# Kernel tuning notes

Measured on AMD Instinct MI355X. Metric: run time of the kernel, lower is better.

The kernel has to match this reference:

```python
import jax, jax.numpy as jnp
import numpy as np

NEG_INF = -jnp.inf
EPS = 1e-12  # F.normalize eps


def _build_spans(text_mask_row, max_span_length):
    # text_mask_row: concrete bool array [S]. Returns static numpy span index arrays.
    pos = np.nonzero(np.asarray(text_mask_row))[0]
    n = pos.size
    starts, ends, lens = [], [], []
    for i in range(n):
        for j in range(i, min(i + max_span_length, n)):
            starts.append(pos[i]); ends.append(pos[j]); lens.append(j - i + 1)
    return (np.asarray(starts, np.int32), np.asarray(ends, np.int32), np.asarray(lens, np.int32))


def setup_inputs() -> dict:
    key = jax.random.key(0)
    ks = jax.random.split(key, 8)
    B, S, H, T = 16, 1024, 768, 64
    L, LE = 4, 32
    Din = 3 * H + LE
    return {
        "hidden_states": jax.random.normal(ks[0], (B, S, H), jnp.float32),
        "topic_hidden": jax.random.normal(ks[1], (B, T, H), jnp.float32),
        "topic_mask": jnp.ones((B, T), jnp.bool_),
        "text_mask": jnp.ones((B, S), jnp.bool_),
        "len_emb": jax.random.normal(ks[2], (L + 1, LE), jnp.float32) * 0.02,
        "W1": jax.random.normal(ks[3], (Din, H), jnp.float32) / np.sqrt(Din),
        "b1": jnp.zeros((H,), jnp.float32),
        "W2": jax.random.normal(ks[4], (H, H), jnp.float32) / np.sqrt(H),
        "b2": jnp.zeros((H,), jnp.float32),
    }


def _l2norm(x):
    n = jnp.sqrt(jnp.sum(x * x, axis=-1, keepdims=True))
    return x / jnp.maximum(n, EPS)


def reference(hidden_states, topic_hidden, topic_mask, text_mask, len_emb, W1, b1, W2, b2):
    B, S, H = hidden_states.shape
    max_span_length = len_emb.shape[0] - 1
    # Masks are identical across the batch (all ones here): build spans once.
    starts_np, ends_np, lens_np = _build_spans(text_mask[0], max_span_length)
    starts = jnp.asarray(starts_np); ends = jnp.asarray(ends_np); lens = jnp.asarray(lens_np)
    N = starts.shape[0]

    start_v = hidden_states[:, starts]          # [B,N,H] gather span starts
    end_v = hidden_states[:, ends]              # [B,N,H] gather span ends
    csum = jnp.concatenate([jnp.zeros((B, 1, H), hidden_states.dtype),
                            jnp.cumsum(hidden_states, axis=1)], axis=1)  # [B,S+1,H]
    mean_v = (csum[:, ends + 1] - csum[:, starts]) / lens[None, :, None].astype(hidden_states.dtype)
    len_v = jnp.broadcast_to(len_emb[lens][None], (B, N, len_emb.shape[1]))

    feat = jnp.concatenate([start_v, end_v, mean_v, len_v], axis=-1)  # [B,N,3H+LE]
    span_vec = jax.nn.gelu(feat @ W1 + b1, approximate=False) @ W2 + b2  # [B,N,H]
    span_vec = _l2norm(span_vec)
    topic_vec = _l2norm(topic_hidden)                                    # [B,T,H]

    sim = jnp.einsum('bth,bnh->btn', topic_vec, span_vec)                # [B,T,N]
    sim = jnp.where(topic_mask[:, :, None], sim, NEG_INF)
    span_scores = jnp.max(sim, axis=1)                                   # [B,N]

    tok = jnp.arange(S)
    cover = (tok[None, :] >= starts[:, None]) & (tok[None, :] <= ends[:, None])  # [N,S]
    token_scores = jnp.max(jnp.where(cover[None], span_scores[:, :, None], NEG_INF), axis=1)  # [B,S]
    token_scores = jnp.where(text_mask, token_scores, NEG_INF)
    return token_scores
```

## Files before the change

kernel.cpp:

```cpp
#include <hip/hip_runtime.h>
#include <hip/hip_bf16.h>
#include <math.h>

typedef __bf16 bf16s;
typedef __attribute__((ext_vector_type(8))) __bf16 bf16x8;
typedef __attribute__((ext_vector_type(4))) __bf16 bf16x4;
typedef __attribute__((ext_vector_type(4))) float f32x4;

#define B_   16
#define S_   1024
#define H_   768
#define T_   64
#define L_   4
#define LE_  32
#define NPAD 4096
#define BS   (B_*S_)
#define BNR  (B_*NPAD)
#define N3   (3*H_)

static __device__ __forceinline__ void gload_lds16(const void* g, void* l) {
  __builtin_amdgcn_global_load_lds(
      (const __attribute__((address_space(1))) void*)g,
      (__attribute__((address_space(3))) void*)l, 16, 0, 0);
}

__global__ __launch_bounds__(1024) void k_build_spans(
    const int* __restrict__ text_mask,
    int* __restrict__ R, int* __restrict__ pos, int* __restrict__ spoff,
    int* __restrict__ starts, int* __restrict__ ends, int* __restrict__ lens,
    int* __restrict__ meta)
{
  __shared__ int buf[S_];
  int t = threadIdx.x;
  int m = text_mask[t] ? 1 : 0;
  buf[t] = m;
  __syncthreads();
  for (int off = 1; off < S_; off <<= 1) {
    int v = buf[t];
    if (t >= off) v += buf[t - off];
    __syncthreads();
    buf[t] = v;
    __syncthreads();
  }
  int incl = buf[t];
  R[t] = incl;
  if (m) pos[incl - 1] = t;
  int n = buf[S_ - 1];
  __syncthreads();
  int cnt = (t < n) ? min(L_, n - t) : 0;
  buf[t] = cnt;
  __syncthreads();
  for (int off = 1; off < S_; off <<= 1) {
    int v = buf[t];
    if (t >= off) v += buf[t - off];
    __syncthreads();
    buf[t] = v;
    __syncthreads();
  }
  int inc2 = buf[t];
  int base = inc2 - cnt;
  spoff[t] = base;
  if (t == 0) { meta[0] = buf[S_ - 1]; meta[1] = n; }
  __syncthreads();
  if (t < n) {
    int p0 = pos[t];
    for (int k = 0; k < cnt; k++) {
      starts[base + k] = p0;
      ends[base + k]   = pos[t + k];
      lens[base + k]   = k + 1;
    }
  }
}

__global__ __launch_bounds__(256) void k_cast_bf16(const float* __restrict__ src,
                                                   bf16s* __restrict__ dst, int n4) {
  int i = blockIdx.x * 256 + threadIdx.x;
  if (i >= n4) return;
  f32x4 v = ((const f32x4*)src)[i];
  bf16x4 o;
  o[0] = (__bf16)v[0]; o[1] = (__bf16)v[1]; o[2] = (__bf16)v[2]; o[3] = (__bf16)v[3];
  ((bf16x4*)dst)[i] = o;
}

__global__ __launch_bounds__(256) void k_zero(float* __restrict__ p, int n4) {
  int i = blockIdx.x * 256 + threadIdx.x;
  if (i < n4) ((f32x4*)p)[i] = (f32x4){0.f, 0.f, 0.f, 0.f};
}

__global__ __launch_bounds__(256) void k_transpose_cast(const float* __restrict__ in,
                                                        bf16s* __restrict__ out) {
  __shared__ float tile[64][65];
  int r0 = blockIdx.x * 64, c0 = blockIdx.y * 64;
  int t = threadIdx.x;
  int tr = t >> 4;
  int tc = (t & 15) * 4;
#pragma unroll
  for (int i = 0; i < 4; i++) {
    int row = tr + i * 16;
    f32x4 v = *(const f32x4*)(in + (long)(r0 + row) * H_ + c0 + tc);
    tile[row][tc+0] = v[0]; tile[row][tc+1] = v[1];
    tile[row][tc+2] = v[2]; tile[row][tc+3] = v[3];
  }
  __syncthreads();
#pragma unroll
  for (int i = 0; i < 4; i++) {
    int cc = tr + i * 16;
    bf16x4 o;
    o[0] = (__bf16)tile[tc+0][cc]; o[1] = (__bf16)tile[tc+1][cc];
    o[2] = (__bf16)tile[tc+2][cc]; o[3] = (__bf16)tile[tc+3][cc];
    *(bf16x4*)(out + (long)(c0 + cc) * H_ + r0 + tc) = o;
  }
}

__global__ __launch_bounds__(256) void k_lt(const float* __restrict__ len_emb,
                                            const float* __restrict__ W1,
                                            float* __restrict__ LT) {
  int idx = blockIdx.x * 256 + threadIdx.x;
  if (idx >= (L_ + 1) * H_) return;
  int l = idx / H_, h = idx % H_;
  float acc = 0.f;
#pragma unroll
  for (int e = 0; e < LE_; e++) acc += len_emb[l * LE_ + e] * W1[(long)(N3 + e) * H_ + h];
  LT[idx] = acc;
}

#define BKT 64
#define GEMM_CORE_BODY(A_, Bt_, K_) \
  int tid = threadIdx.x; \
  int wid = tid >> 6, l = tid & 63; \
  int wr = wid >> 2, wc = wid & 3; \
  int srow = tid >> 3; \
  int sslot = (tid & 7) ^ (srow & 7); \
  const bf16s* gA = (A_) + (a0 + srow) * (long)(K_) + sslot * 8; \
  const bf16s* gB = (Bt_) + (b0 + srow) * (long)(K_) + sslot * 8; \
  const char* aP0 = sA + wr * 16384; \
  const char* aP1 = aP0 + 32768; \
  const char* bP0 = sB + (wc >> 1) * 16384 + (wc & 1) * 8192; \
  const char* bP1 = bP0 + 32768; \
  int lrow = (l & 15) * 128; \
  int ls0 = (((l >> 4) ^ (l & 7)) * 16); \
  f32x4 acc[8][4]; \
  _Pragma("unroll") \
  for (int i = 0; i < 8; i++) \
    _Pragma("unroll") \
    for (int j = 0; j < 4; j++) acc[i][j] = (f32x4){0.f, 0.f, 0.f, 0.f}; \
  int NT = (K_) / BKT; \
  int NITER = NT / 2; \
  STG_B(0, 0); STG_B(0, 1); STG_A(0, 0); STG_A(0, 1); \
  STG_B(1, 0); STG_B(1, 1); STG_A(1, 0); \
  asm volatile("s_waitcnt vmcnt(6)" ::: "memory"); \
  __builtin_amdgcn_s_barrier(); \
  for (int it = 0; it < NITER; ++it) { \
    int t0 = 2 * it, t1 = t0 + 1; \
    bool nl = (it != NITER - 1); \
    bf16x8 af0[4][2], af1[4][2], bfv[4][2]; \
    _Pragma("unroll") \
    for (int f = 0; f < 4; ++f) { \
      af0[f][0] = *(const bf16x8*)(aP0 + f * 2048 + lrow + ls0); \
      af0[f][1] = *(const bf16x8*)(aP0 + f * 2048 + lrow + (ls0 ^ 64)); \
    } \
    _Pragma("unroll") \
    for (int c = 0; c < 4; ++c) { \
      bfv[c][0] = *(const bf16x8*)(bP0 + c * 2048 + lrow + ls0); \
      bfv[c][1] = *(const bf16x8*)(bP0 + c * 2048 + lrow + (ls0 ^ 64)); \
    } \
    STG_A(t1, 1); \
    PH_PRE(); \
    MFMA_Q(af0, 0, 0); MFMA_Q(af0, 0, 1); \
    PH_POST(); \
    if (nl) STG_B(t0 + 2, 0); \
    PH_PRE(); \
    MFMA_Q(af0, 0, 2); MFMA_Q(af0, 0, 3); \
    PH_POST(); \
    _Pragma("unroll") \
    for (int f = 0; f < 4; ++f) { \
      af1[f][0] = *(const bf16x8*)(aP0 + (f + 4) * 2048 + lrow + ls0); \
      af1[f][1] = *(const bf16x8*)(aP0 + (f + 4) * 2048 + lrow + (ls0 ^ 64)); \
    } \
    if (nl) STG_B(t0 + 2, 1); \
    PH_PRE(); \
    MFMA_Q(af1, 4, 0); MFMA_Q(af1, 4, 1); \
    PH_POST(); \
    if (nl) { STG_A(t0 + 2, 0); asm volatile("s_waitcnt vmcnt(6)" ::: "memory"); } \
    else    { asm volatile("s_waitcnt vmcnt(0)" ::: "memory"); } \
    PH_PRE(); \
    MFMA_Q(af1, 4, 2); MFMA_Q(af1, 4, 3); \
    PH_POST(); \
    _Pragma("unroll") \
    for (int f = 0; f < 4; ++f) { \
      af0[f][0] = *(const bf16x8*)(aP1 + f * 2048 + lrow + ls0); \
      af0[f][1] = *(const bf16x8*)(aP1 + f * 2048 + lrow + (ls0 ^ 64)); \
    } \
    _Pragma("unroll") \
    for (int c = 0; c < 4; ++c) { \
      bfv[c][0] = *(const bf16x8*)(bP1 + c * 2048 + lrow + ls0); \
      bfv[c][1] = *(const bf16x8*)(bP1 + c * 2048 + lrow + (ls0 ^ 64)); \
    } \
    if (nl) STG_A(t0 + 2, 1); \
    PH_PRE(); \
    MFMA_Q(af0, 0, 0); MFMA_Q(af0, 0, 1); \
    PH_POST(); \
    if (nl) STG_B(t1 + 2, 0); \
    PH_PRE(); \
    MFMA_Q(af0, 0, 2); MFMA_Q(af0, 0, 3); \
    PH_POST(); \
    _Pragma("unroll") \
    for (int f = 0; f < 4; ++f) { \
      af1[f][0] = *(const bf16x8*)(aP1 + (f + 4) * 2048 + lrow + ls0); \
      af1[f][1] = *(const bf16x8*)(aP1 + (f + 4) * 2048 + lrow + (ls0 ^ 64)); \
    } \
    if (nl) STG_B(t1 + 2, 1); \
    PH_PRE(); \
    MFMA_Q(af1, 4, 0); MFMA_Q(af1, 4, 1); \
    PH_POST(); \
    if (nl) { STG_A(t1 + 2, 0); asm volatile("s_waitcnt vmcnt(6)" ::: "memory"); } \
    else    { asm volatile("s_waitcnt vmcnt(0)" ::: "memory"); } \
    PH_PRE(); \
    MFMA_Q(af1, 4, 2); MFMA_Q(af1, 4, 3); \
    PH_POST(); \
  }

#define STG_A(kt_, h_) do { \
    const bf16s* s_ = gA + (long)(h_) * 128 * K + (long)(kt_) * BKT; \
    char* d_ = sA + ((kt_) & 1) * 32768 + (h_) * 16384 + wid * 1024; \
    gload_lds16(s_, d_); \
    gload_lds16(s_ + 64L * K, d_ + 8192); \
  } while (0)
#define STG_B(kt_, h_) do { \
    const bf16s* s_ = gB + (long)(h_) * 128 * K + (long)(kt_) * BKT; \
    char* d_ = sB + ((kt_) & 1) * 32768 + (h_) * 16384 + wid * 1024; \
    gload_lds16(s_, d_); \
    gload_lds16(s_ + 64L * K, d_ + 8192); \
  } while (0)
#define MFMA_Q(AF_, FR0_, FC_) do { \
    _Pragma("unroll") \
    for (int f_ = 0; f_ < 4; ++f_) { \
      acc[FR0_+f_][FC_] = __builtin_amdgcn_mfma_f32_16x16x32_bf16(bfv[FC_][0], AF_[f_][0], acc[FR0_+f_][FC_], 0, 0, 0); \
      acc[FR0_+f_][FC_] = __builtin_amdgcn_mfma_f32_16x16x32_bf16(bfv[FC_][1], AF_[f_][1], acc[FR0_+f_][FC_], 0, 0, 0); \
    } } while (0)
#define PH_PRE()  __builtin_amdgcn_s_barrier(); \
                  asm volatile("s_waitcnt lgkmcnt(0)" ::: "memory"); \
                  __builtin_amdgcn_s_setprio(1)
#define PH_POST() __builtin_amdgcn_s_setprio(0); \
                  __builtin_amdgcn_s_barrier()

__global__ __launch_bounds__(512, 2) void k_gemm8p(
    const bf16s* __restrict__ A, const bf16s* __restrict__ Bt,
    bf16s* __restrict__ C, int N, int K, int NTN)
{
  __shared__ __align__(16) char sA[65536];
  __shared__ __align__(16) char sB[65536];
  int nwg = gridDim.x, bid = blockIdx.x;
  int q = nwg >> 3, rr = nwg & 7;
  int xcd = bid & 7, ix = bid >> 3;
  int nid = (xcd < rr ? xcd * (q + 1) : rr * (q + 1) + (xcd - rr) * q) + ix;
  long a0 = (long)(nid / NTN) * 256;
  long b0 = (long)(nid % NTN) * 256;

  GEMM_CORE_BODY(A, Bt, K)

#pragma unroll
  for (int half = 0; half < 2; ++half) {
    if (wr == half) {
#pragma unroll
      for (int fc = 0; fc < 4; ++fc) {
        int col2 = (wc * 64 + fc * 16 + (l >> 4) * 4) * 2;
#pragma unroll
        for (int fr = 0; fr < 8; ++fr) {
          int row_l = fr * 16 + (l & 15);
          bf16x4 o;
#pragma unroll
          for (int r = 0; r < 4; ++r) o[r] = (__bf16)acc[fr][fc][r];
          *(bf16x4*)(sA + ((row_l * 512 + col2) ^ ((row_l & 7) << 4))) = o;
        }
      }
    }
    __syncthreads();
#pragma unroll
    for (int i = 0; i < 8; ++i) {
      int off = i * 8192 + tid * 16;
      int row_l = off >> 9;
      bf16x8 v = *(const bf16x8*)(sA + (off ^ ((row_l & 7) << 4)));
      *(bf16x8*)(C + (a0 + half * 128 + row_l) * (long)N + b0 + ((off & 511) >> 1)) = v;
    }
    __syncthreads();
  }
}

__global__ __launch_bounds__(512, 2) void k_gemmnorm(
    const bf16s* __restrict__ A, const bf16s* __restrict__ Bt,
    const float* __restrict__ bias, float* __restrict__ ssbuf,
    int K, int NTN)
{
  __shared__ __align__(16) char sA[65536];
  __shared__ __align__(16) char sB[65536];
  int nwg = gridDim.x, bid = blockIdx.x;
  int q = nwg >> 3, rr = nwg & 7;
  int xcd = bid & 7, ix = bid >> 3;
  int nid = (xcd < rr ? xcd * (q + 1) : rr * (q + 1) + (xcd - rr) * q) + ix;
  long a0 = (long)(nid / NTN) * 256;
  long b0 = (long)(nid % NTN) * 256;

  GEMM_CORE_BODY(A, Bt, K)

  f32x4 bb[4];
#pragma unroll
  for (int fc = 0; fc < 4; ++fc)
    bb[fc] = *(const f32x4*)(bias + b0 + wc * 64 + fc * 16 + (l >> 4) * 4);
#pragma unroll
  for (int fr = 0; fr < 8; ++fr) {
    float p = 0.f;
#pragma unroll
    for (int fc = 0; fc < 4; ++fc)
#pragma unroll
      for (int r = 0; r < 4; ++r) {
        float y = acc[fr][fc][r] + bb[fc][r];
        p += y * y;
      }
    p += __shfl_xor(p, 16);
    p += __shfl_xor(p, 32);
    if (l < 16) atomicAdd(&ssbuf[a0 + wr * 128 + fr * 16 + l], p);
  }
}

#undef STG_A
#undef STG_B
#undef MFMA_Q
#undef PH_PRE
#undef PH_POST

__global__ __launch_bounds__(256) void k_z1(
    const bf16s* __restrict__ P,
    const float* __restrict__ LT, const float* __restrict__ b1,
    const int* __restrict__ starts, const int* __restrict__ ends,
    const int* __restrict__ lens, const int* __restrict__ meta,
    bf16s* __restrict__ X)
{
  int idx = blockIdx.x * 256 + threadIdx.x;
  int h4 = idx % (H_ / 4); int rest = idx / (H_ / 4);
  int nid = rest % NPAD; int b = rest / NPAD;
  int h = h4 * 4;
  int N = meta[0];
  long orow = (long)(b * NPAD + nid) * H_ + h;
  if (nid >= N) {
    bf16x4 z; z[0] = z[1] = z[2] = z[3] = (__bf16)0.f;
    *(bf16x4*)(X + orow) = z;
    return;
  }
  int sa = starts[nid], se = ends[nid], ln = lens[nid];
  float il = 1.0f / (float)ln;
  bf16x4 vs = *(const bf16x4*)(P + (long)(b * S_ + sa) * N3 + h);
  bf16x4 ve = *(const bf16x4*)(P + (long)(b * S_ + se) * N3 + H_ + h);
  float mv[4] = {0.f, 0.f, 0.f, 0.f};
  for (int i = sa; i <= se; i++) {
    bf16x4 vc = *(const bf16x4*)(P + (long)(b * S_ + i) * N3 + 2 * H_ + h);
#pragma unroll
    for (int j = 0; j < 4; j++) mv[j] += (float)vc[j];
  }
  f32x4 lt = *(const f32x4*)(LT + (long)ln * H_ + h);
  f32x4 bb = *(const f32x4*)(b1 + h);
  bf16x4 o;
#pragma unroll
  for (int j = 0; j < 4; j++) {
    float x = (float)vs[j] + (float)ve[j] + mv[j] * il + lt[j] + bb[j];
    float g = 0.5f * x * (1.0f + erff(x * 0.70710678118654752f));
    o[j] = (__bf16)g;
  }
  *(bf16x4*)(X + orow) = o;
}

__global__ __launch_bounds__(256) void k_topicn(const float* __restrict__ TH,
                                                const float* __restrict__ b2,
                                                bf16s* __restrict__ TN,
                                                float* __restrict__ cvec) {
  __shared__ float red[256];
  int r = blockIdx.x; int t = threadIdx.x;
  const float* row = TH + (long)r * H_;
  float v0 = row[t], v1 = row[t + 256], v2 = row[t + 512];
  red[t] = v0 * v0 + v1 * v1 + v2 * v2;
  __syncthreads();
  for (int off = 128; off; off >>= 1) {
    if (t < off) red[t] += red[t + off];
    __syncthreads();
  }
  float rn = 1.0f / fmaxf(sqrtf(red[0]), 1e-12f);
  bf16s* o = TN + (long)r * H_;
  o[t] = (__bf16)(v0 * rn); o[t + 256] = (__bf16)(v1 * rn); o[t + 512] = (__bf16)(v2 * rn);
  __syncthreads();
  red[t] = v0 * b2[t] + v1 * b2[t + 256] + v2 * b2[t + 512];
  __syncthreads();
  for (int off = 128; off; off >>= 1) {
    if (t < off) red[t] += red[t + off];
    __syncthreads();
  }
  if (t == 0) cvec[r] = red[0] * rn;
}

__global__ __launch_bounds__(256) void k_simx(
    const bf16s* __restrict__ X, const bf16s* __restrict__ U,
    const float* __restrict__ cvec, const float* __restrict__ ssbuf,
    const int* __restrict__ tmask, float* __restrict__ scores)
{
  int b = blockIdx.y;
  int wid = threadIdx.x >> 6, l = threadIdx.x & 63;
  int st = blockIdx.x * 4 + wid;
  int span = st * 16 + (l & 15);
  const bf16s* xrow = X + (long)(b * NPAD + span) * H_ + (l >> 4) * 8;
  const bf16s* ubase = U + (long)b * T_ * H_ + (l >> 4) * 8;
  f32x4 acc[4];
#pragma unroll
  for (int tt = 0; tt < 4; tt++) acc[tt] = (f32x4){0.f, 0.f, 0.f, 0.f};
  for (int kk = 0; kk < H_ / 32; kk++) {
    bf16x8 av = *(const bf16x8*)(xrow + kk * 32);
#pragma unroll
    for (int tt = 0; tt < 4; tt++) {
      bf16x8 bv = *(const bf16x8*)(ubase + (long)(tt * 16 + (l & 15)) * H_ + kk * 32);
      acc[tt] = __builtin_amdgcn_mfma_f32_16x16x32_bf16(av, bv, acc[tt], 0, 0, 0);
    }
  }
  const int* tm = tmask + b * T_;
  bool msk[4];
  float cv[4];
#pragma unroll
  for (int tt = 0; tt < 4; tt++) {
    int tcol = tt * 16 + (l & 15);
    msk[tt] = tm[tcol] != 0;
    cv[tt] = cvec[b * T_ + tcol];
  }
  float best[4];
#pragma unroll
  for (int r = 0; r < 4; r++) {
    float v = -INFINITY;
#pragma unroll
    for (int tt = 0; tt < 4; tt++) if (msk[tt]) v = fmaxf(v, acc[tt][r] + cv[tt]);
    best[r] = v;
  }
#pragma unroll
  for (int off = 8; off; off >>= 1)
#pragma unroll
    for (int r = 0; r < 4; r++) best[r] = fmaxf(best[r], __shfl_xor(best[r], off));
  if ((l & 15) == 0) {
    int srow = st * 16 + (l >> 4) * 4;
#pragma unroll
    for (int r = 0; r < 4; r++) {
      float ss = ssbuf[b * NPAD + srow + r];
      scores[b * NPAD + srow + r] = best[r] / fmaxf(sqrtf(ss), 1e-12f);
    }
  }
}

__global__ __launch_bounds__(256) void k_token(
    const int* __restrict__ text_mask,
    const int* __restrict__ R, const int* __restrict__ spoff,
    const int* __restrict__ meta, const float* __restrict__ scores,
    float* __restrict__ out)
{
  int idx = blockIdx.x * 256 + threadIdx.x;
  int s = idx % S_, b = idx / S_;
  if (!text_mask[b * S_ + s]) { out[idx] = -INFINITY; return; }
  int n = meta[1];
  int r1 = R[s];
  int le = r1 - 1;
  int ge = text_mask[s] ? (r1 - 1) : r1;
  float best = -INFINITY;
  if (le >= 0 && ge < n) {
    int i0 = max(0, ge - (L_ - 1));
    for (int i = i0; i <= le; i++) {
      int jmax = min(i + L_ - 1, n - 1);
      int off = spoff[i];
      for (int j = max(i, ge); j <= jmax; j++)
        best = fmaxf(best, scores[b * NPAD + off + (j - i)]);
    }
  }
  out[idx] = best;
}

__global__ __launch_bounds__(256) void k_sentinel(float* __restrict__ out) {
  int i = blockIdx.x * 256 + threadIdx.x;
  if (i < BS) out[i] = 12345.0f;
}

extern "C" void kernel_launch(void* const* d_in, const int* in_sizes, int n_in,
                              void* d_out, int out_size, void* d_ws, size_t ws_size,
                              hipStream_t stream) {
  const float* hid = (const float*)d_in[0];
  const float* th  = (const float*)d_in[1];
  const int* tmask = (const int*)d_in[2];
  const int* xmask = (const int*)d_in[3];
  const float* lemb = (const float*)d_in[4];
  const float* W1   = (const float*)d_in[5];
  const float* b1   = (const float*)d_in[6];
  const float* W2   = (const float*)d_in[7];
  const float* b2   = (const float*)d_in[8];
  float* out = (float*)d_out;

  char* w = (char*)d_ws;
  auto alloc = [&](size_t bytes) {
    char* p = w; w += (bytes + 255) & ~(size_t)255; return p;
  };
  bf16s* wbt   = (bf16s*)alloc((size_t)N3 * H_ * 2);
  bf16s* w2t   = (bf16s*)alloc((size_t)H_ * H_ * 2);
  bf16s* w2c   = (bf16s*)alloc((size_t)H_ * H_ * 2);
  float* LT    = (float*)alloc((size_t)(L_ + 1) * H_ * 4);
  bf16s* topn  = (bf16s*)alloc((size_t)B_ * T_ * H_ * 2);
  bf16s* U     = (bf16s*)alloc((size_t)B_ * T_ * H_ * 2);
  float* cvec  = (float*)alloc((size_t)B_ * T_ * 4);
  float* ssbuf = (float*)alloc((size_t)BNR * 4);
  float* scores= (float*)alloc((size_t)B_ * NPAD * 4);
  int* R       = (int*)alloc(S_ * 4);
  int* pos     = (int*)alloc(S_ * 4);
  int* spoff   = (int*)alloc(S_ * 4);
  int* starts  = (int*)alloc(NPAD * 4);
  int* ends    = (int*)alloc(NPAD * 4);
  int* lens    = (int*)alloc(NPAD * 4);
  int* meta    = (int*)alloc(2 * 4);
  char* regionA = alloc((size_t)BS * H_ * 2 + (size_t)BS * N3 * 2);
  bf16s* hidb  = (bf16s*)regionA;
  bf16s* P     = (bf16s*)(regionA + (size_t)BS * H_ * 2);
  bf16s* X     = (bf16s*)alloc((size_t)BNR * H_ * 2);

  size_t required = (size_t)(w - (char*)d_ws);
  if (required > ws_size) {
    k_sentinel<<<(BS + 255) / 256, 256, 0, stream>>>(out);
    return;
  }

  k_build_spans<<<1, 1024, 0, stream>>>(xmask, R, pos, spoff, starts, ends, lens, meta);
  k_cast_bf16<<<(BS * H_ / 4 + 255) / 256, 256, 0, stream>>>(hid, hidb, BS * H_ / 4);
  for (int c = 0; c < 3; c++)
    k_transpose_cast<<<dim3(12, 12), 256, 0, stream>>>(W1 + (size_t)c * H_ * H_, wbt + (size_t)c * H_ * H_);
  k_transpose_cast<<<dim3(12, 12), 256, 0, stream>>>(W2, w2t);
  k_cast_bf16<<<(H_ * H_ / 4 + 255) / 256, 256, 0, stream>>>(W2, w2c, H_ * H_ / 4);
  k_lt<<<((L_ + 1) * H_ + 255) / 256, 256, 0, stream>>>(lemb, W1, LT);
  k_zero<<<(BNR / 4 + 255) / 256, 256, 0, stream>>>(ssbuf, BNR / 4);

  k_gemm8p<<<(BS / 256) * (N3 / 256), 512, 0, stream>>>(hidb, wbt, P, N3, H_, N3 / 256);

  k_z1<<<(B_ * NPAD * (H_ / 4)) / 256, 256, 0, stream>>>(P, LT, b1, starts, ends, lens, meta, X);

  k_topicn<<<B_ * T_, 256, 0, stream>>>(th, b2, topn, cvec);
  k_gemm8p<<<(B_ * T_ / 256) * (H_ / 256), 512, 0, stream>>>(topn, w2c, U, H_, H_, H_ / 256);

  k_gemmnorm<<<(BNR / 256) * (H_ / 256), 512, 0, stream>>>(X, w2t, b2, ssbuf, H_, H_ / 256);

  k_simx<<<dim3(NPAD / 64, B_), 256, 0, stream>>>(X, U, cvec, ssbuf, tmask, scores);
  k_token<<<(B_ * S_) / 256, 256, 0, stream>>>(xmask, R, spoff, meta, scores, out);
  (void)in_sizes; (void)n_in; (void)out_size;
}
```

Measured before the change: 348.2 us.

## Merge prep kernels, chain GEMM column tiles per block, drop atomics and zeroing

New measurement: 322.1 us. -7.5%, faster.

```diff
diff --git a/kernel.cpp b/kernel.cpp
--- a/kernel.cpp
+++ b/kernel.cpp
@@ -72,162 +72,95 @@
   }
 }
 
-__global__ __launch_bounds__(256) void k_cast_bf16(const float* __restrict__ src,
-                                                   bf16s* __restrict__ dst, int n4) {
-  int i = blockIdx.x * 256 + threadIdx.x;
-  if (i >= n4) return;
-  f32x4 v = ((const f32x4*)src)[i];
-  bf16x4 o;
-  o[0] = (__bf16)v[0]; o[1] = (__bf16)v[1]; o[2] = (__bf16)v[2]; o[3] = (__bf16)v[3];
-  ((bf16x4*)dst)[i] = o;
-}
-
-__global__ __launch_bounds__(256) void k_zero(float* __restrict__ p, int n4) {
-  int i = blockIdx.x * 256 + threadIdx.x;
-  if (i < n4) ((f32x4*)p)[i] = (f32x4){0.f, 0.f, 0.f, 0.f};
-}
-
-__global__ __launch_bounds__(256) void k_transpose_cast(const float* __restrict__ in,
-                                                        bf16s* __restrict__ out) {
+__global__ __launch_bounds__(256) void k_prep(
+    const float* __restrict__ hid, bf16s* __restrict__ hidb,
+    const float* __restrict__ W1, bf16s* __restrict__ wbt,
+    const float* __restrict__ W2, bf16s* __restrict__ w2t, bf16s* __restrict__ w2c,
+    const float* __restrict__ lemb, float* __restrict__ LT,
+    const float* __restrict__ TH, const float* __restrict__ b2,
+    bf16s* __restrict__ TN, float* __restrict__ cvec)
+{
   __shared__ float tile[64][65];
-  int r0 = blockIdx.x * 64, c0 = blockIdx.y * 64;
+  __shared__ float red[256];
+  int bid = blockIdx.x;
   int t = threadIdx.x;
-  int tr = t >> 4;
-  int tc = (t & 15) * 4;
-#pragma unroll
-  for (int i = 0; i < 4; i++) {
-    int row = tr + i * 16;
-    f32x4 v = *(const f32x4*)(in + (long)(r0 + row) * H_ + c0 + tc);
-    tile[row][tc+0] = v[0]; tile[row][tc+1] = v[1];
-    tile[row][tc+2] = v[2]; tile[row][tc+3] = v[3];
-  }
-  __syncthreads();
-#pragma unroll
-  for (int i = 0; i < 4; i++) {
-    int cc = tr + i * 16;
+  if (bid < 12288) {
+    int i = bid * 256 + t;
+    f32x4 v = ((const f32x4*)hid)[i];
     bf16x4 o;
-    o[0] = (__bf16)tile[tc+0][cc]; o[1] = (__bf16)tile[tc+1][cc];
-    o[2] = (__bf16)tile[tc+2][cc]; o[3] = (__bf16)tile[tc+3][cc];
-    *(bf16x4*)(out + (long)(c0 + cc) * H_ + r0 + tc) = o;
-  }
-}
-
-__global__ __launch_bounds__(256) void k_lt(const float* __restrict__ len_emb,
-                                            const float* __restrict__ W1,
-                                            float* __restrict__ LT) {
-  int idx = blockIdx.x * 256 + threadIdx.x;
-  if (idx >= (L_ + 1) * H_) return;
-  int l = idx / H_, h = idx % H_;
-  float acc = 0.f;
-#pragma unroll
-  for (int e = 0; e < LE_; e++) acc += len_emb[l * LE_ + e] * W1[(long)(N3 + e) * H_ + h];
-  LT[idx] = acc;
+    o[0] = (__bf16)v[0]; o[1] = (__bf16)v[1]; o[2] = (__bf16)v[2]; o[3] = (__bf16)v[3];
+    ((bf16x4*)hidb)[i] = o;
+  } else if (bid < 12864) {
+    int local = bid - 12288;
+    int c = local / 144, rem = local % 144;
+    const float* in = (c < 3) ? (W1 + (size_t)c * H_ * H_) : W2;
+    bf16s* out = (c < 3) ? (wbt + (size_t)c * H_ * H_) : w2t;
+    int r0 = (rem / 12) * 64, c0 = (rem % 12) * 64;
+    int tr = t >> 4, tc = (t & 15) * 4;
+#pragma unroll
+    for (int i = 0; i < 4; i++) {
+      int row = tr + i * 16;
+      f32x4 v = *(const f32x4*)(in + (long)(r0 + row) * H_ + c0 + tc);
+      tile[row][tc+0] = v[0]; tile[row][tc+1] = v[1];
+      tile[row][tc+2] = v[2]; tile[row][tc+3] = v[3];
+    }
+    __syncthreads();
+#pragma unroll
+    for (int i = 0; i < 4; i++) {
+      int cc = tr + i * 16;
+      bf16x4 o;
+      o[0] = (__bf16)tile[tc+0][cc]; o[1] = (__bf16)tile[tc+1][cc];
+      o[2] = (__bf16)tile[tc+2][cc]; o[3] = (__bf16)tile[tc+3][cc];
+      *(bf16x4*)(out + (long)(c0 + cc) * H_ + r0 + tc) = o;
+    }
+  } else if (bid < 13440) {
+    int i = (bid - 12864) * 256 + t;
+    f32x4 v = ((const f32x4*)W2)[i];
+    bf16x4 o;
+    o[0] = (__bf16)v[0]; o[1] = (__bf16)v[1]; o[2] = (__bf16)v[2]; o[3] = (__bf16)v[3];
+    ((bf16x4*)w2c)[i] = o;
+  } else if (bid < 13455) {
+    int idx = (bid - 13440) * 256 + t;
+    if (idx < (L_ + 1) * H_) {
+      int l = idx / H_, h = idx % H_;
+      float acc = 0.f;
+#pragma unroll
+      for (int e = 0; e < LE_; e++) acc += lemb[l * LE_ + e] * W1[(long)(N3 + e) * H_ + h];
+      LT[idx] = acc;
+    }
+  } else {
+    int r = bid - 13455;
+    const float* row = TH + (long)r * H_;
+    float v0 = row[t], v1 = row[t + 256], v2 = row[t + 512];
+    red[t] = v0 * v0 + v1 * v1 + v2 * v2;
+    __syncthreads();
+    for (int off = 128; off; off >>= 1) {
+      if (t < off) red[t] += red[t + off];
+      __syncthreads();
+    }
+    float rn = 1.0f / fmaxf(sqrtf(red[0]), 1e-12f);
+    bf16s* o = TN + (long)r * H_;
+    o[t] = (__bf16)(v0 * rn); o[t + 256] = (__bf16)(v1 * rn); o[t + 512] = (__bf16)(v2 * rn);
+    __syncthreads();
+    red[t] = v0 * b2[t] + v1 * b2[t + 256] + v2 * b2[t + 512];
+    __syncthreads();
+    for (int off = 128; off; off >>= 1) {
+      if (t < off) red[t] += red[t + off];
+      __syncthreads();
+    }
+    if (t == 0) cvec[r] = red[0] * rn;
+  }
 }
 
 #define BKT 64
-#define GEMM_CORE_BODY(A_, Bt_, K_) \
-  int tid = threadIdx.x; \
-  int wid = tid >> 6, l = tid & 63; \
-  int wr = wid >> 2, wc = wid & 3; \
-  int srow = tid >> 3; \
-  int sslot = (tid & 7) ^ (srow & 7); \
-  const bf16s* gA = (A_) + (a0 + srow) * (long)(K_) + sslot * 8; \
-  const bf16s* gB = (Bt_) + (b0 + srow) * (long)(K_) + sslot * 8; \
-  const char* aP0 = sA + wr * 16384; \
-  const char* aP1 = aP0 + 32768; \
-  const char* bP0 = sB + (wc >> 1) * 16384 + (wc & 1) * 8192; \
-  const char* bP1 = bP0 + 32768; \
-  int lrow = (l & 15) * 128; \
-  int ls0 = (((l >> 4) ^ (l & 7)) * 16); \
-  f32x4 acc[8][4]; \
-  _Pragma("unroll") \
-  for (int i = 0; i < 8; i++) \
-    _Pragma("unroll") \
-    for (int j = 0; j < 4; j++) acc[i][j] = (f32x4){0.f, 0.f, 0.f, 0.f}; \
-  int NT = (K_) / BKT; \
-  int NITER = NT / 2; \
-  STG_B(0, 0); STG_B(0, 1); STG_A(0, 0); STG_A(0, 1); \
-  STG_B(1, 0); STG_B(1, 1); STG_A(1, 0); \
-  asm volatile("s_waitcnt vmcnt(6)" ::: "memory"); \
-  __builtin_amdgcn_s_barrier(); \
-  for (int it = 0; it < NITER; ++it) { \
-    int t0 = 2 * it, t1 = t0 + 1; \
-    bool nl = (it != NITER - 1); \
-    bf16x8 af0[4][2], af1[4][2], bfv[4][2]; \
-    _Pragma("unroll") \
-    for (int f = 0; f < 4; ++f) { \
-      af0[f][0] = *(const bf16x8*)(aP0 + f * 2048 + lrow + ls0); \
-      af0[f][1] = *(const bf16x8*)(aP0 + f * 2048 + lrow + (ls0 ^ 64)); \
-    } \
-    _Pragma("unroll") \
-    for (int c = 0; c < 4; ++c) { \
-      bfv[c][0] = *(const bf16x8*)(bP0 + c * 2048 + lrow + ls0); \
-      bfv[c][1] = *(const bf16x8*)(bP0 + c * 2048 + lrow + (ls0 ^ 64)); \
-    } \
-    STG_A(t1, 1); \
-    PH_PRE(); \
-    MFMA_Q(af0, 0, 0); MFMA_Q(af0, 0, 1); \
-    PH_POST(); \
-    if (nl) STG_B(t0 + 2, 0); \
-    PH_PRE(); \
-    MFMA_Q(af0, 0, 2); MFMA_Q(af0, 0, 3); \
-    PH_POST(); \
-    _Pragma("unroll") \
-    for (int f = 0; f < 4; ++f) { \
-      af1[f][0] = *(const bf16x8*)(aP0 + (f + 4) * 2048 + lrow + ls0); \
-      af1[f][1] = *(const bf16x8*)(aP0 + (f + 4) * 2048 + lrow + (ls0 ^ 64)); \
-    } \
-    if (nl) STG_B(t0 + 2, 1); \
-    PH_PRE(); \
-    MFMA_Q(af1, 4, 0); MFMA_Q(af1, 4, 1); \
-    PH_POST(); \
-    if (nl) { STG_A(t0 + 2, 0); asm volatile("s_waitcnt vmcnt(6)" ::: "memory"); } \
-    else    { asm volatile("s_waitcnt vmcnt(0)" ::: "memory"); } \
-    PH_PRE(); \
-    MFMA_Q(af1, 4, 2); MFMA_Q(af1, 4, 3); \
-    PH_POST(); \
-    _Pragma("unroll") \
-    for (int f = 0; f < 4; ++f) { \
-      af0[f][0] = *(const bf16x8*)(aP1 + f * 2048 + lrow + ls0); \
-      af0[f][1] = *(const bf16x8*)(aP1 + f * 2048 + lrow + (ls0 ^ 64)); \
-    } \
-    _Pragma("unroll") \
-    for (int c = 0; c < 4; ++c) { \
-      bfv[c][0] = *(const bf16x8*)(bP1 + c * 2048 + lrow + ls0); \
-      bfv[c][1] = *(const bf16x8*)(bP1 + c * 2048 + lrow + (ls0 ^ 64)); \
-    } \
-    if (nl) STG_A(t0 + 2, 1); \
-    PH_PRE(); \
-    MFMA_Q(af0, 0, 0); MFMA_Q(af0, 0, 1); \
-    PH_POST(); \
-    if (nl) STG_B(t1 + 2, 0); \
-    PH_PRE(); \
-    MFMA_Q(af0, 0, 2); MFMA_Q(af0, 0, 3); \
-    PH_POST(); \
-    _Pragma("unroll") \
-    for (int f = 0; f < 4; ++f) { \
-      af1[f][0] = *(const bf16x8*)(aP1 + (f + 4) * 2048 + lrow + ls0); \
-      af1[f][1] = *(const bf16x8*)(aP1 + (f + 4) * 2048 + lrow + (ls0 ^ 64)); \
-    } \
-    if (nl) STG_B(t1 + 2, 1); \
-    PH_PRE(); \
-    MFMA_Q(af1, 4, 0); MFMA_Q(af1, 4, 1); \
-    PH_POST(); \
-    if (nl) { STG_A(t1 + 2, 0); asm volatile("s_waitcnt vmcnt(6)" ::: "memory"); } \
-    else    { asm volatile("s_waitcnt vmcnt(0)" ::: "memory"); } \
-    PH_PRE(); \
-    MFMA_Q(af1, 4, 2); MFMA_Q(af1, 4, 3); \
-    PH_POST(); \
-  }
-
 #define STG_A(kt_, h_) do { \
     const bf16s* s_ = gA + (long)(h_) * 128 * K + (long)(kt_) * BKT; \
     char* d_ = sA + ((kt_) & 1) * 32768 + (h_) * 16384 + wid * 1024; \
     gload_lds16(s_, d_); \
     gload_lds16(s_ + 64L * K, d_ + 8192); \
   } while (0)
-#define STG_B(kt_, h_) do { \
-    const bf16s* s_ = gB + (long)(h_) * 128 * K + (long)(kt_) * BKT; \
+#define STG_B(ct_, kt_, h_) do { \
+    const bf16s* s_ = gB + (long)(ct_) * 256 * K + (long)(h_) * 128 * K + (long)(kt_) * BKT; \
     char* d_ = sB + ((kt_) & 1) * 32768 + (h_) * 16384 + wid * 1024; \
     gload_lds16(s_, d_); \
     gload_lds16(s_ + 64L * K, d_ + 8192); \
@@ -244,85 +177,236 @@
 #define PH_POST() __builtin_amdgcn_s_setprio(0); \
                   __builtin_amdgcn_s_barrier()
 
-__global__ __launch_bounds__(512, 2) void k_gemm8p(
-    const bf16s* __restrict__ A, const bf16s* __restrict__ Bt,
-    bf16s* __restrict__ C, int N, int K, int NTN)
+#define CHAIN_CORE(EPILOG_) \
+  const char* aP0 = sA + wr * 16384; \
+  const char* aP1 = aP0 + 32768; \
+  const char* bP0 = sB + (wc >> 1) * 16384 + (wc & 1) * 8192; \
+  const char* bP1 = bP0 + 32768; \
+  int lrow = (l & 15) * 128; \
+  int ls0 = (((l >> 4) ^ (l & 7)) * 16); \
+  f32x4 acc[8][4]; \
+  _Pragma("unroll") \
+  for (int i_ = 0; i_ < 8; i_++) \
+    _Pragma("unroll") \
+    for (int j_ = 0; j_ < 4; j_++) acc[i_][j_] = (f32x4){0.f, 0.f, 0.f, 0.f}; \
+  STG_B(0, 0, 0); STG_B(0, 0, 1); STG_A(0, 0); STG_A(0, 1); \
+  STG_B(0, 1, 0); STG_B(0, 1, 1); STG_A(1, 0); \
+  asm volatile("s_waitcnt vmcnt(6)" ::: "memory"); \
+  __builtin_amdgcn_s_barrier(); \
+  for (int s = 0; s < 3; ++s) { \
+    for (int it = 0; it < 6; ++it) { \
+      int kt0 = 2 * it; \
+      bool nl = !(s == 2 && it == 5); \
+      int ctn = (it == 5) ? s + 1 : s; \
+      int kn0 = (it == 5) ? 0 : kt0 + 2; \
+      int kn1 = (it == 5) ? 1 : kt0 + 3; \
+      bf16x8 af0[4][2], af1[4][2], bfv[4][2]; \
+       \
+      _Pragma("unroll") \
+      for (int f = 0; f < 4; ++f) { \
+        af0[f][0] = *(const bf16x8*)(aP0 + f * 2048 + lrow + ls0); \
+        af0[f][1] = *(const bf16x8*)(aP0 + f * 2048 + lrow + (ls0 ^ 64)); \
+      } \
+      _Pragma("unroll") \
+      for (int c = 0; c < 4; ++c) { \
+        bfv[c][0] = *(const bf16x8*)(bP0 + c * 2048 + lrow + ls0); \
+        bfv[c][1] = *(const bf16x8*)(bP0 + c * 2048 + lrow + (ls0 ^ 64)); \
+      } \
+      STG_A(kt0 + 1, 1); \
+      PH_PRE(); \
+      MFMA_Q(af0, 0, 0); MFMA_Q(af0, 0, 1); \
+      PH_POST(); \
+       \
+      if (nl) STG_B(ctn, kn0, 0); \
+      PH_PRE(); \
+      MFMA_Q(af0, 0, 2); MFMA_Q(af0, 0, 3); \
+      PH_POST(); \
+       \
+      _Pragma("unroll") \
+      for (int f = 0; f < 4; ++f) { \
+        af1[f][0] = *(const bf16x8*)(aP0 + (f + 4) * 2048 + lrow + ls0); \
+        af1[f][1] = *(const bf16x8*)(aP0 + (f + 4) * 2048 + lrow + (ls0 ^ 64)); \
+      } \
+      if (nl) STG_B(ctn, kn0, 1); \
+      PH_PRE(); \
+      MFMA_Q(af1, 4, 0); MFMA_Q(af1, 4, 1); \
+      PH_POST(); \
+       \
+      if (nl) { STG_A(kn0, 0); asm volatile("s_waitcnt vmcnt(6)" ::: "memory"); } \
+      else    { asm volatile("s_waitcnt vmcnt(0)" ::: "memory"); } \
+      PH_PRE(); \
+      MFMA_Q(af1, 4, 2); MFMA_Q(af1, 4, 3); \
+      PH_POST(); \
+       \
+      _Pragma("unroll") \
+      for (int f = 0; f < 4; ++f) { \
+        af0[f][0] = *(const bf16x8*)(aP1 + f * 2048 + lrow + ls0); \
+        af0[f][1] = *(const bf16x8*)(aP1 + f * 2048 + lrow + (ls0 ^ 64)); \
+      } \
+      _Pragma("unroll") \
+      for (int c = 0; c < 4; ++c) { \
+        bfv[c][0] = *(const bf16x8*)(bP1 + c * 2048 + lrow + ls0); \
+        bfv[c][1] = *(const bf16x8*)(bP1 + c * 2048 + lrow + (ls0 ^ 64)); \
+      } \
+      if (nl) STG_A(kn0, 1); \
+      PH_PRE(); \
+      MFMA_Q(af0, 0, 0); MFMA_Q(af0, 0, 1); \
+      PH_POST(); \
+       \
+      if (nl) STG_B(ctn, kn1, 0); \
+      PH_PRE(); \
+      MFMA_Q(af0, 0, 2); MFMA_Q(af0, 0, 3); \
+      PH_POST(); \
+       \
+      _Pragma("unroll") \
+      for (int f = 0; f < 4; ++f) { \
+        af1[f][0] = *(const bf16x8*)(aP1 + (f + 4) * 2048 + lrow + ls0); \
+        af1[f][1] = *(const bf16x8*)(aP1 + (f + 4) * 2048 + lrow + (ls0 ^ 64)); \
+      } \
+      if (nl) STG_B(ctn, kn1, 1); \
+      PH_PRE(); \
+      MFMA_Q(af1, 4, 0); MFMA_Q(af1, 4, 1); \
+      PH_POST(); \
+       \
+      if (nl) { STG_A(kn1, 0); asm volatile("s_waitcnt vmcnt(6)" ::: "memory"); } \
+      else    { asm volatile("s_waitcnt vmcnt(0)" ::: "memory"); } \
+      PH_PRE(); \
+      MFMA_Q(af1, 4, 2); MFMA_Q(af1, 4, 3); \
+      PH_POST(); \
+    } \
+    EPILOG_(s); \
+  }
+
+__global__ __launch_bounds__(512, 1) void k_gemm1u(
+    const bf16s* __restrict__ Ah, const bf16s* __restrict__ Bth, bf16s* __restrict__ Ch,
+    const bf16s* __restrict__ Au, const bf16s* __restrict__ Btu, bf16s* __restrict__ Cu)
 {
   __shared__ __align__(16) char sA[65536];
   __shared__ __align__(16) char sB[65536];
-  int nwg = gridDim.x, bid = blockIdx.x;
-  int q = nwg >> 3, rr = nwg & 7;
-  int xcd = bid & 7, ix = bid >> 3;
-  int nid = (xcd < rr ? xcd * (q + 1) : rr * (q + 1) + (xcd - rr) * q) + ix;
-  long a0 = (long)(nid / NTN) * 256;
-  long b0 = (long)(nid % NTN) * 256;
-
-  GEMM_CORE_BODY(A, Bt, K)
-
-#pragma unroll
-  for (int half = 0; half < 2; ++half) {
-    if (wr == half) {
-#pragma unroll
-      for (int fc = 0; fc < 4; ++fc) {
-        int col2 = (wc * 64 + fc * 16 + (l >> 4) * 4) * 2;
-#pragma unroll
-        for (int fr = 0; fr < 8; ++fr) {
-          int row_l = fr * 16 + (l & 15);
-          bf16x4 o;
-#pragma unroll
-          for (int r = 0; r < 4; ++r) o[r] = (__bf16)acc[fr][fc][r];
-          *(bf16x4*)(sA + ((row_l * 512 + col2) ^ ((row_l & 7) << 4))) = o;
-        }
-      }
-    }
-    __syncthreads();
-#pragma unroll
-    for (int i = 0; i < 8; ++i) {
-      int off = i * 8192 + tid * 16;
-      int row_l = off >> 9;
-      bf16x8 v = *(const bf16x8*)(sA + (off ^ ((row_l & 7) << 4)));
-      *(bf16x8*)(C + (a0 + half * 128 + row_l) * (long)N + b0 + ((off & 511) >> 1)) = v;
-    }
-    __syncthreads();
-  }
-}
-
-__global__ __launch_bounds__(512, 2) void k_gemmnorm(
-    const bf16s* __restrict__ A, const bf16s* __restrict__ Bt,
-    const float* __restrict__ bias, float* __restrict__ ssbuf,
-    int K, int NTN)
+  __shared__ __align__(16) char sC[16384];
+  const int K = H_;
+  int bid = blockIdx.x;
+  const bf16s *A, *Bt;
+  bf16s* C;
+  long a0, b0base;
+  int NN;
+  if (bid < 192) {
+    int nid = (bid & 7) * 24 + (bid >> 3);
+    A = Ah; Bt = Bth; C = Ch; NN = N3;
+    a0 = (long)(nid / 3) * 256;
+    b0base = (long)(nid % 3) * 768;
+  } else {
+    A = Au; Bt = Btu; C = Cu; NN = H_;
+    a0 = (long)(bid - 192) * 256;
+    b0base = 0;
+  }
+  int tid = threadIdx.x;
+  int wid = tid >> 6, l = tid & 63;
+  int wr = wid >> 2, wc = wid & 3;
+  int srow = tid >> 3;
+  int sslot = (tid & 7) ^ (srow & 7);
+  const bf16s* gA = A + (a0 + srow) * (long)K + sslot * 8;
+  const bf16s* gB = Bt + (b0base + srow) * (long)K + sslot * 8;
+
+#define EPI_C(s_) do { \
+    long cb = b0base + (s_) * 256; \
+    _Pragma("unroll") \
+    for (int e = 0; e < 8; ++e) { \
+      if (wr == (e >> 2)) { \
+        int f0 = (e & 3) * 2; \
+        _Pragma("unroll") \
+        for (int ff = 0; ff < 2; ++ff) { \
+          int fr = f0 + ff; \
+          int row_l = ff * 16 + (l & 15); \
+          _Pragma("unroll") \
+          for (int fc = 0; fc < 4; ++fc) { \
+            int col2 = (wc * 64 + fc * 16 + (l >> 4) * 4) * 2; \
+            bf16x4 o; \
+            _Pragma("unroll") \
+            for (int r = 0; r < 4; ++r) o[r] = (__bf16)acc[fr][fc][r]; \
+            *(bf16x4*)(sC + ((row_l * 512 + col2) ^ ((row_l & 7) << 4))) = o; \
+          } \
+        } \
+      } \
+      __syncthreads(); \
+      _Pragma("unroll") \
+      for (int pp = 0; pp < 2; ++pp) { \
+        int off = pp * 8192 + tid * 16; \
+        int row_l = off >> 9; \
+        bf16x8 v = *(const bf16x8*)(sC + (off ^ ((row_l & 7) << 4))); \
+        *(bf16x8*)(C + (a0 + e * 32 + row_l) * (long)NN + cb + ((off & 511) >> 1)) = v; \
+      } \
+      __syncthreads(); \
+    } \
+    _Pragma("unroll") \
+    for (int i_ = 0; i_ < 8; i_++) \
+      _Pragma("unroll") \
+      for (int j_ = 0; j_ < 4; j_++) acc[i_][j_] = (f32x4){0.f, 0.f, 0.f, 0.f}; \
+  } while (0)
+
+  CHAIN_CORE(EPI_C)
+#undef EPI_C
+}
+
+__global__ __launch_bounds__(512, 1) void k_gemmnorm(
+    const bf16s* __restrict__ Ax, const bf16s* __restrict__ Btw,
+    const float* __restrict__ bias, float* __restrict__ ssbuf)
 {
   __shared__ __align__(16) char sA[65536];
   __shared__ __align__(16) char sB[65536];
-  int nwg = gridDim.x, bid = blockIdx.x;
-  int q = nwg >> 3, rr = nwg & 7;
-  int xcd = bid & 7, ix = bid >> 3;
-  int nid = (xcd < rr ? xcd * (q + 1) : rr * (q + 1) + (xcd - rr) * q) + ix;
-  long a0 = (long)(nid / NTN) * 256;
-  long b0 = (long)(nid % NTN) * 256;
-
-  GEMM_CORE_BODY(A, Bt, K)
-
-  f32x4 bb[4];
-#pragma unroll
-  for (int fc = 0; fc < 4; ++fc)
-    bb[fc] = *(const f32x4*)(bias + b0 + wc * 64 + fc * 16 + (l >> 4) * 4);
+  const int K = H_;
+  int bid = blockIdx.x;
+  int nid = (bid & 7) * 32 + (bid >> 3);
+  long a0 = (long)nid * 256;
+  long b0base = 0;
+  int tid = threadIdx.x;
+  int wid = tid >> 6, l = tid & 63;
+  int wr = wid >> 2, wc = wid & 3;
+  int srow = tid >> 3;
+  int sslot = (tid & 7) ^ (srow & 7);
+  const bf16s* gA = Ax + (a0 + srow) * (long)K + sslot * 8;
+  const bf16s* gB = Btw + (b0base + srow) * (long)K + sslot * 8;
+  float ssp[8] = {0.f, 0.f, 0.f, 0.f, 0.f, 0.f, 0.f, 0.f};
+
+#define EPI_N(s_) do { \
+    f32x4 bb[4]; \
+    _Pragma("unroll") \
+    for (int fc = 0; fc < 4; ++fc) \
+      bb[fc] = *(const f32x4*)(bias + (s_) * 256 + wc * 64 + fc * 16 + (l >> 4) * 4); \
+    _Pragma("unroll") \
+    for (int fr = 0; fr < 8; ++fr) { \
+      float p = 0.f; \
+      _Pragma("unroll") \
+      for (int fc = 0; fc < 4; ++fc) { \
+        _Pragma("unroll") \
+        for (int r = 0; r < 4; ++r) { \
+          float y = acc[fr][fc][r] + bb[fc][r]; \
+          p += y * y; \
+        } \
+        acc[fr][fc] = (f32x4){0.f, 0.f, 0.f, 0.f}; \
+      } \
+      ssp[fr] += p; \
+    } \
+  } while (0)
+
+  CHAIN_CORE(EPI_N)
+#undef EPI_N
+
+  float* sred = (float*)sA;
 #pragma unroll
   for (int fr = 0; fr < 8; ++fr) {
-    float p = 0.f;
-#pragma unroll
-    for (int fc = 0; fc < 4; ++fc)
-#pragma unroll
-      for (int r = 0; r < 4; ++r) {
-        float y = acc[fr][fc][r] + bb[fc][r];
-        p += y * y;
-      }
+    float p = ssp[fr];
     p += __shfl_xor(p, 16);
     p += __shfl_xor(p, 32);
-    if (l < 16) atomicAdd(&ssbuf[a0 + wr * 128 + fr * 16 + l], p);
-  }
-}
-
+    if (l < 16) sred[wc * 256 + wr * 128 + fr * 16 + l] = p;
+  }
+  __syncthreads();
+  if (tid < 256) {
+    ssbuf[a0 + tid] = sred[tid] + sred[256 + tid] + sred[512 + tid] + sred[768 + tid];
+  }
+}
+
+#undef CHAIN_CORE
 #undef STG_A
 #undef STG_B
 #undef MFMA_Q
@@ -337,63 +421,42 @@
     bf16s* __restrict__ X)
 {
   int idx = blockIdx.x * 256 + threadIdx.x;
-  int h4 = idx % (H_ / 4); int rest = idx / (H_ / 4);
+  int h8 = idx % 96; int rest = idx / 96;
   int nid = rest % NPAD; int b = rest / NPAD;
-  int h = h4 * 4;
+  int h = h8 * 8;
   int N = meta[0];
   long orow = (long)(b * NPAD + nid) * H_ + h;
   if (nid >= N) {
-    bf16x4 z; z[0] = z[1] = z[2] = z[3] = (__bf16)0.f;
-    *(bf16x4*)(X + orow) = z;
+    bf16x8 z;
+#pragma unroll
+    for (int j = 0; j < 8; j++) z[j] = (__bf16)0.f;
+    *(bf16x8*)(X + orow) = z;
     return;
   }
   int sa = starts[nid], se = ends[nid], ln = lens[nid];
   float il = 1.0f / (float)ln;
-  bf16x4 vs = *(const bf16x4*)(P + (long)(b * S_ + sa) * N3 + h);
-  bf16x4 ve = *(const bf16x4*)(P + (long)(b * S_ + se) * N3 + H_ + h);
-  float mv[4] = {0.f, 0.f, 0.f, 0.f};
+  bf16x8 vs = *(const bf16x8*)(P + (long)(b * S_ + sa) * N3 + h);
+  bf16x8 ve = *(const bf16x8*)(P + (long)(b * S_ + se) * N3 + H_ + h);
+  float mv[8] = {0.f, 0.f, 0.f, 0.f, 0.f, 0.f, 0.f, 0.f};
   for (int i = sa; i <= se; i++) {
-    bf16x4 vc = *(const bf16x4*)(P + (long)(b * S_ + i) * N3 + 2 * H_ + h);
-#pragma unroll
-    for (int j = 0; j < 4; j++) mv[j] += (float)vc[j];
-  }
-  f32x4 lt = *(const f32x4*)(LT + (long)ln * H_ + h);
-  f32x4 bb = *(const f32x4*)(b1 + h);
-  bf16x4 o;
-#pragma unroll
-  for (int j = 0; j < 4; j++) {
-    float x = (float)vs[j] + (float)ve[j] + mv[j] * il + lt[j] + bb[j];
+    bf16x8 vc = *(const bf16x8*)(P + (long)(b * S_ + i) * N3 + 2 * H_ + h);
+#pragma unroll
+    for (int j = 0; j < 8; j++) mv[j] += (float)vc[j];
+  }
+  f32x4 lt0 = *(const f32x4*)(LT + (long)ln * H_ + h);
+  f32x4 lt1 = *(const f32x4*)(LT + (long)ln * H_ + h + 4);
+  f32x4 bb0 = *(const f32x4*)(b1 + h);
+  f32x4 bb1 = *(const f32x4*)(b1 + h + 4);
+  bf16x8 o;
+#pragma unroll
+  for (int j = 0; j < 8; j++) {
+    float ltv = (j < 4) ? lt0[j] : lt1[j - 4];
+    float bbv = (j < 4) ? bb0[j] : bb1[j - 4];
+    float x = (float)vs[j] + (float)ve[j] + mv[j] * il + ltv + bbv;
     float g = 0.5f * x * (1.0f + erff(x * 0.70710678118654752f));
     o[j] = (__bf16)g;
   }
-  *(bf16x4*)(X + orow) = o;
-}
-
-__global__ __launch_bounds__(256) void k_topicn(const float* __restrict__ TH,
-                                                const float* __restrict__ b2,
-                                                bf16s* __restrict__ TN,
-                                                float* __restrict__ cvec) {
-  __shared__ float red[256];
-  int r = blockIdx.x; int t = threadIdx.x;
-  const float* row = TH + (long)r * H_;
-  float v0 = row[t], v1 = row[t + 256], v2 = row[t + 512];
-  red[t] = v0 * v0 + v1 * v1 + v2 * v2;
-  __syncthreads();
-  for (int off = 128; off; off >>= 1) {
-    if (t < off) red[t] += red[t + off];
-    __syncthreads();
-  }
-  float rn = 1.0f / fmaxf(sqrtf(red[0]), 1e-12f);
-  bf16s* o = TN + (long)r * H_;
-  o[t] = (__bf16)(v0 * rn); o[t + 256] = (__bf16)(v1 * rn); o[t + 512] = (__bf16)(v2 * rn);
-  __syncthreads();
-  red[t] = v0 * b2[t] + v1 * b2[t + 256] + v2 * b2[t + 512];
-  __syncthreads();
-  for (int off = 128; off; off >>= 1) {
-    if (t < off) red[t] += red[t + off];
-    __syncthreads();
-  }
-  if (t == 0) cvec[r] = red[0] * rn;
+  *(bf16x8*)(X + orow) = o;
 }
 
 __global__ __launch_bounds__(256) void k_simx(
@@ -526,22 +589,14 @@
   }
 
   k_build_spans<<<1, 1024, 0, stream>>>(xmask, R, pos, spoff, starts, ends, lens, meta);
-  k_cast_bf16<<<(BS * H_ / 4 + 255) / 256, 256, 0, stream>>>(hid, hidb, BS * H_ / 4);
-  for (int c = 0; c < 3; c++)
-    k_transpose_cast<<<dim3(12, 12), 256, 0, stream>>>(W1 + (size_t)c * H_ * H_, wbt + (size_t)c * H_ * H_);
-  k_transpose_cast<<<dim3(12, 12), 256, 0, stream>>>(W2, w2t);
-  k_cast_bf16<<<(H_ * H_ / 4 + 255) / 256, 256, 0, stream>>>(W2, w2c, H_ * H_ / 4);
-  k_lt<<<((L_ + 1) * H_ + 255) / 256, 256, 0, stream>>>(lemb, W1, LT);
-  k_zero<<<(BNR / 4 + 255) / 256, 256, 0, stream>>>(ssbuf, BNR / 4);
-
-  k_gemm8p<<<(BS / 256) * (N3 / 256), 512, 0, stream>>>(hidb, wbt, P, N3, H_, N3 / 256);
-
-  k_z1<<<(B_ * NPAD * (H_ / 4)) / 256, 256, 0, stream>>>(P, LT, b1, starts, ends, lens, meta, X);
-
-  k_topicn<<<B_ * T_, 256, 0, stream>>>(th, b2, topn, cvec);
-  k_gemm8p<<<(B_ * T_ / 256) * (H_ / 256), 512, 0, stream>>>(topn, w2c, U, H_, H_, H_ / 256);
-
-  k_gemmnorm<<<(BNR / 256) * (H_ / 256), 512, 0, stream>>>(X, w2t, b2, ssbuf, H_, H_ / 256);
+  k_prep<<<14479, 256, 0, stream>>>(hid, hidb, W1, wbt, W2, w2t, w2c,
+                                    lemb, LT, th, b2, topn, cvec);
+
+  k_gemm1u<<<196, 512, 0, stream>>>(hidb, wbt, P, topn, w2c, U);
+
+  k_z1<<<(BNR * 96) / 256, 256, 0, stream>>>(P, LT, b1, starts, ends, lens, meta, X);
+
+  k_gemmnorm<<<256, 512, 0, stream>>>(X, w2t, b2, ssbuf);
 
   k_simx<<<dim3(NPAD / 64, B_), 256, 0, stream>>>(X, U, cvec, ssbuf, tmask, scores);
   k_token<<<(B_ * S_) / 256, 256, 0, stream>>>(xmask, R, spoff, meta, scores, out);
```
